# Performance work log

Measured on AMD Instinct MI355X. Metric: run time of the kernel, lower is better.

Reference implementation:

```python
import jax, jax.numpy as jnp
from jax import lax
import numpy as np

EPS = 1e-5
NEG_SLOPE = 0.1
POOL = 2


def _cond_block(x, w, b, fcw, fcb, g, be, rm, rv):
    """CondConv1d(k=3,pad=1,num_experts=e) + BatchNorm1d(eval) + LeakyReLU(0.1).
    x: (B, Cin, W); w: (E, Cout, Cin, 3); b: (E, Cout); fcw: (E, Cin); fcb: (E,)
    """
    # routing: adaptive avg pool to 1 -> fc -> sigmoid  => (B, E)
    r = jax.nn.sigmoid(x.mean(axis=-1) @ fcw.T + fcb)
    # per-sample mixed weights/bias
    cw = jnp.einsum('be,eoik->boik', r, w)          # (B, Cout, Cin, 3)
    cb = r @ b                                      # (B, Cout)
    # batched per-sample conv1d (same padding, stride 1)
    def one(xi, wi):
        return lax.conv_general_dilated(
            xi[None], wi, window_strides=(1,), padding=[(1, 1)],
            dimension_numbers=('NCH', 'OIH', 'NCH'))[0]
    y = jax.vmap(one)(x, cw) + cb[:, :, None]       # (B, Cout, W)
    # BatchNorm1d in eval mode (running stats)
    y = (y - rm[None, :, None]) * (g[None, :, None] / jnp.sqrt(rv[None, :, None] + EPS)) + be[None, :, None]
    # LeakyReLU(0.1)
    return jnp.where(y >= 0, y, NEG_SLOPE * y)


def setup_inputs() -> dict:
    key = jax.random.key(0)
    ks = jax.random.split(key, 16)
    B, W = 32, 2048
    chans = [64, 128, 256]
    E = 1  # num_experts default
    inp = {'x': jax.random.normal(ks[0], (B, chans[0], W), dtype=jnp.float32)}
    i = 1
    for li, (ci, co) in enumerate(zip(chans[:-1], chans[1:]), start=1):
        fan_in = ci * 3
        wb = float(np.sqrt(6.0 / fan_in))  # kaiming_uniform a=sqrt(5) scale approx
        bb = float(1.0 / np.sqrt(fan_in))
        inp[f'w{li}'] = jax.random.uniform(ks[i], (E, co, ci, 3), minval=-wb, maxval=wb, dtype=jnp.float32); i += 1
        inp[f'b{li}'] = jax.random.uniform(ks[i], (E, co), minval=-bb, maxval=bb, dtype=jnp.float32); i += 1
        inp[f'fcw{li}'] = jax.random.normal(ks[i], (E, ci), dtype=jnp.float32) * 0.05; i += 1
        inp[f'fcb{li}'] = jnp.zeros((E,), dtype=jnp.float32)
        inp[f'g{li}'] = 1.0 + 0.1 * jax.random.normal(ks[i], (co,), dtype=jnp.float32); i += 1
        inp[f'be{li}'] = 0.1 * jax.random.normal(ks[i], (co,), dtype=jnp.float32); i += 1
        inp[f'rm{li}'] = 0.1 * jax.random.normal(ks[i], (co,), dtype=jnp.float32); i += 1
        inp[f'rv{li}'] = 0.5 + jax.random.uniform(ks[i], (co,), dtype=jnp.float32); i += 1
    return inp


def reference(x, w1, b1, fcw1, fcb1, g1, be1, rm1, rv1,
              w2, b2, fcw2, fcb2, g2, be2, rm2, rv2):
    y = _cond_block(x, w1, b1, fcw1, fcb1, g1, be1, rm1, rv1)
    y = _cond_block(y, w2, b2, fcw2, fcb2, g2, be2, rm2, rv2)
    # max_pool1d(kernel=stride=POOL)
    B, C, W = y.shape
    y = y.reshape(B, C, W // POOL, POOL).max(axis=-1)
    # dropout: eval mode -> identity
    return y
```

## Files before the change

kernel.cpp:

```cpp
#include <hip/hip_runtime.h>
#include <hip/hip_bf16.h>
#include <math.h>

#define BATCH 32
#define WLEN  2048

typedef __attribute__((ext_vector_type(8))) short short8;
typedef __attribute__((ext_vector_type(4))) short short4v;
typedef __attribute__((ext_vector_type(4))) float floatx4;

__device__ inline short f2bf(float f) {
  unsigned u = __float_as_uint(f);
  unsigned r = (u + 0x7fffu + ((u >> 16) & 1u)) >> 16;
  return (short)r;
}

__global__ __launch_bounds__(256) void fused_prep(
    const float* __restrict__ w1, const float* __restrict__ w2,
    const float* __restrict__ x, const float* __restrict__ fcw1,
    short* __restrict__ wp1, short* __restrict__ wp2,
    float* __restrict__ racc1) {
  const int blk = blockIdx.x;
  const int tid = threadIdx.x;
  if (blk < 12) {
    int iw = blk * 256 + tid;
    int o = iw & 127;
    int t = iw >> 7;
    int ig = t & 7;
    int k = t >> 3;
    short8 v;
#pragma unroll
    for (int e = 0; e < 8; ++e) v[e] = f2bf(w1[(o * 64 + ig * 8 + e) * 3 + k]);
    *(short8*)(wp1 + (size_t)iw * 8) = v;
  } else if (blk < 60) {
    int iw = (blk - 12) * 256 + tid;
    int o = iw & 255;
    int t = iw >> 8;
    int ig = t & 15;
    int k = t >> 4;
    short8 v;
#pragma unroll
    for (int e = 0; e < 8; ++e) v[e] = f2bf(w2[(o * 128 + ig * 8 + e) * 3 + k]);
    *(short8*)(wp2 + (size_t)iw * 8) = v;
  } else {
    int t = blk - 60;
    int j = t & 7, b = t >> 3;
    const float4* xb = (const float4*)(x + ((size_t)b * 64 + j * 8) * WLEN);
    float sum = 0.f;
    for (int idx = tid; idx < 8 * 512; idx += 256) {
      int c = idx >> 9;
      float4 v = xb[idx];
      sum += (v.x + v.y + v.z + v.w) * fcw1[j * 8 + c];
    }
    __shared__ float red[256];
    red[tid] = sum;
    __syncthreads();
    for (int s = 128; s > 0; s >>= 1) {
      if (tid < s) red[tid] += red[tid + s];
      __syncthreads();
    }
    if (tid == 0) racc1[b * 8 + j] = red[0];
  }
}

__global__ __launch_bounds__(512) void conv1_mfma(
    const float* __restrict__ x, const short* __restrict__ wp1,
    const float* __restrict__ bias, const float* __restrict__ g,
    const float* __restrict__ be, const float* __restrict__ rm,
    const float* __restrict__ rv, const float* __restrict__ racc1,
    const float* __restrict__ fcb, const float* __restrict__ fcw2,
    short* __restrict__ y1p, float* __restrict__ racc2) {
  const int b = blockIdx.y;
  const int w_base = blockIdx.x * 128;
  const int tid = threadIdx.x;
  const int wave = tid >> 6, lane = tid & 63;
  const int ln = lane & 15, kg = lane >> 4;
  const int oh = wave & 1, wq = wave >> 1;

  __shared__ short xs[8 * 130 * 8];
  __shared__ float red[512];

  const float* xb = x + (size_t)b * 64 * WLEN;
  for (int idx = tid; idx < 8 * 130; idx += 512) {
    int ig = idx / 130;
    int p = idx - ig * 130;
    int w = w_base - 1 + p;
    short8 v = {0, 0, 0, 0, 0, 0, 0, 0};
    if ((unsigned)w < (unsigned)WLEN) {
      const float* src = xb + (size_t)(ig * 8) * WLEN + w;
#pragma unroll
      for (int e = 0; e < 8; ++e) v[e] = f2bf(src[(size_t)e * WLEN]);
    }
    *(short8*)(xs + idx * 8) = v;
  }
  __syncthreads();

  floatx4 acc[4][2];
#pragma unroll
  for (int ms = 0; ms < 4; ++ms)
#pragma unroll
    for (int ns = 0; ns < 2; ++ns) acc[ms][ns] = (floatx4){0.f, 0.f, 0.f, 0.f};

#pragma unroll
  for (int q = 0; q < 2; ++q) {
#pragma unroll
    for (int k = 0; k < 3; ++k) {
      short8 af[4];
      const short* wk =
          wp1 + ((size_t)(k * 8 + q * 4 + kg) * 128 + oh * 64 + ln) * 8;
#pragma unroll
      for (int ms = 0; ms < 4; ++ms)
        af[ms] = *(const short8*)(wk + (size_t)ms * 16 * 8);
#pragma unroll
      for (int ns = 0; ns < 2; ++ns) {
        short8 bf = *(const short8*)(
            xs + ((q * 4 + kg) * 130 + wq * 32 + ns * 16 + ln + k) * 8);
#pragma unroll
        for (int ms = 0; ms < 4; ++ms)
          acc[ms][ns] = __builtin_amdgcn_mfma_f32_16x16x32_bf16(
              af[ms], bf, acc[ms][ns], 0, 0, 0);
      }
    }
  }

  float zs = 0.f;
#pragma unroll
  for (int qq = 0; qq < 8; ++qq) zs += racc1[b * 8 + qq];
  float z = zs * (1.f / (float)WLEN) + fcb[0];
  float r = 1.f / (1.f + expf(-z));

  float rsum = 0.f;
#pragma unroll
  for (int ms = 0; ms < 4; ++ms) {
    const int o0 = oh * 64 + ms * 16 + kg * 4;
    float a_[4], c_[4], fw[4];
#pragma unroll
    for (int rr = 0; rr < 4; ++rr) {
      int o = o0 + rr;
      float s = g[o] * rsqrtf(rv[o] + 1e-5f);
      a_[rr] = r * s;
      c_[rr] = (r * bias[o] - rm[o]) * s + be[o];
      fw[rr] = fcw2[o];
    }
#pragma unroll
    for (int ns = 0; ns < 2; ++ns) {
      int w = w_base + wq * 32 + ns * 16 + ln;
      short4v pk;
#pragma unroll
      for (int rr = 0; rr < 4; ++rr) {
        float v = acc[ms][ns][rr] * a_[rr] + c_[rr];
        v = v >= 0.f ? v : 0.1f * v;
        rsum += v * fw[rr];
        pk[rr] = f2bf(v);
      }
      *(short4v*)(y1p + ((size_t)(b * 32 + (o0 >> 2)) * WLEN + w) * 4) = pk;
    }
  }

  red[tid] = rsum;
  __syncthreads();
  for (int s = 256; s > 0; s >>= 1) {
    if (tid < s) red[tid] += red[tid + s];
    __syncthreads();
  }
  if (tid == 0) racc2[b * 16 + blockIdx.x] = red[0];
}

__global__ __launch_bounds__(512) void conv2_mfma(
    const short* __restrict__ y1p, const short* __restrict__ wp2,
    const float* __restrict__ bias, const float* __restrict__ g,
    const float* __restrict__ be, const float* __restrict__ rm,
    const float* __restrict__ rv, const float* __restrict__ racc2,
    const float* __restrict__ fcb, float* __restrict__ out) {
  const int b = blockIdx.y;
  const int w_base = blockIdx.x * 128;
  const int tid = threadIdx.x;
  const int wave = tid >> 6, lane = tid & 63;
  const int ln = lane & 15, kg = lane >> 4;
  const int oq = wave & 3, wh = wave >> 2;

  __shared__ short xs[16 * 130 * 8];

  const short* yb = y1p + (size_t)b * 32 * WLEN * 4;
  for (int idx = tid; idx < 16 * 130; idx += 512) {
    int ig = idx / 130;
    int p = idx - ig * 130;
    int w = w_base - 1 + p;
    short8 v = {0, 0, 0, 0, 0, 0, 0, 0};
    if ((unsigned)w < (unsigned)WLEN) {
      short4v a = *(const short4v*)(yb + ((size_t)(ig * 2) * WLEN + w) * 4);
      short4v c = *(const short4v*)(yb + ((size_t)(ig * 2 + 1) * WLEN + w) * 4);
      v[0] = a[0]; v[1] = a[1]; v[2] = a[2]; v[3] = a[3];
      v[4] = c[0]; v[5] = c[1]; v[6] = c[2]; v[7] = c[3];
    }
    *(short8*)(xs + idx * 8) = v;
  }
  __syncthreads();

  floatx4 acc[4][4];
#pragma unroll
  for (int ms = 0; ms < 4; ++ms)
#pragma unroll
    for (int ns = 0; ns < 4; ++ns) acc[ms][ns] = (floatx4){0.f, 0.f, 0.f, 0.f};

#pragma unroll
  for (int q = 0; q < 4; ++q) {
#pragma unroll
    for (int k = 0; k < 3; ++k) {
      short8 af[4];
      const short* wk =
          wp2 + ((size_t)(k * 16 + q * 4 + kg) * 256 + oq * 64 + ln) * 8;
#pragma unroll
      for (int ms = 0; ms < 4; ++ms)
        af[ms] = *(const short8*)(wk + (size_t)ms * 16 * 8);
#pragma unroll
      for (int ns = 0; ns < 4; ++ns) {
        short8 bf = *(const short8*)(
            xs + ((q * 4 + kg) * 130 + wh * 64 + ns * 16 + ln + k) * 8);
#pragma unroll
        for (int ms = 0; ms < 4; ++ms)
          acc[ms][ns] = __builtin_amdgcn_mfma_f32_16x16x32_bf16(
              af[ms], bf, acc[ms][ns], 0, 0, 0);
      }
    }
  }

  float zs = 0.f;
#pragma unroll
  for (int t = 0; t < 16; ++t) zs += racc2[b * 16 + t];
  float z = zs * (1.f / (float)WLEN) + fcb[0];
  float r = 1.f / (1.f + expf(-z));

#pragma unroll
  for (int ms = 0; ms < 4; ++ms) {
    const int o0 = oq * 64 + ms * 16 + kg * 4;
    float a_[4], c_[4];
#pragma unroll
    for (int rr = 0; rr < 4; ++rr) {
      int o = o0 + rr;
      float s = g[o] * rsqrtf(rv[o] + 1e-5f);
      a_[rr] = r * s;
      c_[rr] = (r * bias[o] - rm[o]) * s + be[o];
    }
#pragma unroll
    for (int np = 0; np < 2; ++np) {
      float m0[4], m1[4];
#pragma unroll
      for (int half = 0; half < 2; ++half) {
        int ns = np * 2 + half;
#pragma unroll
        for (int rr = 0; rr < 4; ++rr) {
          float v = acc[ms][ns][rr] * a_[rr] + c_[rr];
          v = v >= 0.f ? v : 0.1f * v;
          float m = fmaxf(v, __shfl_xor(v, 1));
          if (half == 0) m0[rr] = m; else m1[rr] = m;
        }
      }
      const int pc = (w_base >> 1) + wh * 32 + np * 16 + ln;
#pragma unroll
      for (int rr = 0; rr < 4; ++rr) {
        int src = kg * 16 + ((ln & 7) << 1);
        float aa = __shfl(m0[rr], src);
        float bb = __shfl(m1[rr], src);
        float val = (ln < 8) ? aa : bb;
        out[((size_t)(b * 256 + o0 + rr)) * (WLEN / 2) + pc] = val;
      }
    }
  }
}

extern "C" void kernel_launch(void* const* d_in, const int* in_sizes, int n_in,
                              void* d_out, int out_size, void* d_ws, size_t ws_size,
                              hipStream_t stream) {
  const float* x    = (const float*)d_in[0];
  const float* w1   = (const float*)d_in[1];
  const float* b1   = (const float*)d_in[2];
  const float* fcw1 = (const float*)d_in[3];
  const float* fcb1 = (const float*)d_in[4];
  const float* g1   = (const float*)d_in[5];
  const float* be1  = (const float*)d_in[6];
  const float* rm1  = (const float*)d_in[7];
  const float* rv1  = (const float*)d_in[8];
  const float* w2   = (const float*)d_in[9];
  const float* b2   = (const float*)d_in[10];
  const float* fcw2 = (const float*)d_in[11];
  const float* fcb2 = (const float*)d_in[12];
  const float* g2   = (const float*)d_in[13];
  const float* be2  = (const float*)d_in[14];
  const float* rm2  = (const float*)d_in[15];
  const float* rv2  = (const float*)d_in[16];

  float* out = (float*)d_out;

  char* ws = (char*)d_ws;
  short* y1p = (short*)ws;
  short* wp1 = (short*)(ws + (size_t)16 * 1024 * 1024);
  short* wp2 = (short*)(ws + (size_t)16 * 1024 * 1024 + 64 * 1024);
  float* racc1 = (float*)(ws + (size_t)16 * 1024 * 1024 + 512 * 1024);
  float* racc2 = racc1 + 256;

  fused_prep<<<316, 256, 0, stream>>>(w1, w2, x, fcw1, wp1, wp2, racc1);
  conv1_mfma<<<dim3(16, 32), 512, 0, stream>>>(
      x, wp1, b1, g1, be1, rm1, rv1, racc1, fcb1, fcw2, y1p, racc2);
  conv2_mfma<<<dim3(16, 32), 512, 0, stream>>>(
      y1p, wp2, b2, g2, be2, rm2, rv2, racc2, fcb2, out);
}
```

Before: 57.54 us.

## Fuse prep and both conv stages into one cooperative kernel with grid syncs

```diff
diff --git a/kernel.cpp b/kernel.cpp
--- a/kernel.cpp
+++ b/kernel.cpp
@@ -1,6 +1,9 @@
 #include <hip/hip_runtime.h>
 #include <hip/hip_bf16.h>
+#include <hip/hip_cooperative_groups.h>
 #include <math.h>
+
+namespace cg = cooperative_groups;
 
 #define BATCH 32
 #define WLEN  2048
@@ -13,6 +16,273 @@
   unsigned u = __float_as_uint(f);
   unsigned r = (u + 0x7fffu + ((u >> 16) & 1u)) >> 16;
   return (short)r;
+}
+
+__global__ __launch_bounds__(512) void fused_all(
+    const float* __restrict__ x,
+    const float* __restrict__ w1, const float* __restrict__ b1,
+    const float* __restrict__ fcw1, const float* __restrict__ fcb1,
+    const float* __restrict__ g1, const float* __restrict__ be1,
+    const float* __restrict__ rm1, const float* __restrict__ rv1,
+    const float* __restrict__ w2, const float* __restrict__ b2,
+    const float* __restrict__ fcw2, const float* __restrict__ fcb2,
+    const float* __restrict__ g2, const float* __restrict__ be2,
+    const float* __restrict__ rm2, const float* __restrict__ rv2,
+    short* __restrict__ wp1, short* __restrict__ wp2,
+    float* __restrict__ racc1, float* __restrict__ racc2,
+    short* __restrict__ edges, float* __restrict__ out) {
+  const int j = blockIdx.x;
+  const int b = blockIdx.y;
+  const int bid = b * 8 + j;
+  const int tid = threadIdx.x;
+  const int wave = tid >> 6, lane = tid & 63;
+  const int ln = lane & 15, kg = lane >> 4;
+
+  __shared__ short buf[2][16640];
+  __shared__ float red[512];
+
+  cg::grid_group grid = cg::this_grid();
+
+  if (bid < 6) {
+    int iw = bid * 512 + tid;
+    int o = iw & 127;
+    int tt = iw >> 7;
+    int ig = tt & 7;
+    int k = tt >> 3;
+    short8 v;
+#pragma unroll
+    for (int e = 0; e < 8; ++e) v[e] = f2bf(w1[(o * 64 + ig * 8 + e) * 3 + k]);
+    *(short8*)(wp1 + (size_t)iw * 8) = v;
+  } else if (bid < 30) {
+    int iw = (bid - 6) * 512 + tid;
+    int o = iw & 255;
+    int tt = iw >> 8;
+    int ig = tt & 15;
+    int k = tt >> 4;
+    short8 v;
+#pragma unroll
+    for (int e = 0; e < 8; ++e) v[e] = f2bf(w2[(o * 128 + ig * 8 + e) * 3 + k]);
+    *(short8*)(wp2 + (size_t)iw * 8) = v;
+  }
+
+  {
+    const float* xb = x + (size_t)b * 64 * WLEN;
+    float rsum = 0.f;
+#pragma unroll
+    for (int u = 0; u < 2; ++u) {
+      const int w0 = j * 256 + u * 128;
+      for (int idx = tid; idx < 8 * 130; idx += 512) {
+        int ig = idx / 130;
+        int p = idx - ig * 130;
+        int w = w0 - 1 + p;
+        short8 v = {0, 0, 0, 0, 0, 0, 0, 0};
+        if ((unsigned)w < (unsigned)WLEN) {
+          const float* src = xb + (size_t)(ig * 8) * WLEN + w;
+          float fv[8];
+#pragma unroll
+          for (int e = 0; e < 8; ++e) fv[e] = src[(size_t)e * WLEN];
+#pragma unroll
+          for (int e = 0; e < 8; ++e) v[e] = f2bf(fv[e]);
+          if (p >= 1 && p <= 128) {
+#pragma unroll
+            for (int e = 0; e < 8; ++e) rsum += fv[e] * fcw1[ig * 8 + e];
+          }
+        }
+        *(short8*)(buf[u] + (size_t)idx * 8) = v;
+      }
+    }
+    red[tid] = rsum;
+    __syncthreads();
+    for (int s = 256; s > 0; s >>= 1) {
+      if (tid < s) red[tid] += red[tid + s];
+      __syncthreads();
+    }
+    if (tid == 0) racc1[bid] = red[0];
+  }
+  __threadfence();
+  grid.sync();
+
+  {
+    float zs = 0.f;
+#pragma unroll
+    for (int tt = 0; tt < 8; ++tt) zs += racc1[b * 8 + tt];
+    float z = zs * (1.f / (float)WLEN) + fcb1[0];
+    float r1v = 1.f / (1.f + expf(-z));
+
+    const int oh = wave & 1, wq = wave >> 1;
+    float rsum2 = 0.f;
+#pragma unroll
+    for (int u = 0; u < 2; ++u) {
+      floatx4 acc[4][2];
+#pragma unroll
+      for (int ms = 0; ms < 4; ++ms)
+#pragma unroll
+        for (int ns = 0; ns < 2; ++ns) acc[ms][ns] = (floatx4){0.f, 0.f, 0.f, 0.f};
+
+#pragma unroll
+      for (int q = 0; q < 2; ++q) {
+#pragma unroll
+        for (int k = 0; k < 3; ++k) {
+          short8 af[4];
+          const short* wk =
+              wp1 + ((size_t)(k * 8 + q * 4 + kg) * 128 + oh * 64 + ln) * 8;
+#pragma unroll
+          for (int ms = 0; ms < 4; ++ms)
+            af[ms] = *(const short8*)(wk + (size_t)ms * 16 * 8);
+#pragma unroll
+          for (int ns = 0; ns < 2; ++ns) {
+            short8 bf = *(const short8*)(
+                buf[u] + ((q * 4 + kg) * 130 + wq * 32 + ns * 16 + ln + k) * 8);
+#pragma unroll
+            for (int ms = 0; ms < 4; ++ms)
+              acc[ms][ns] = __builtin_amdgcn_mfma_f32_16x16x32_bf16(
+                  af[ms], bf, acc[ms][ns], 0, 0, 0);
+          }
+        }
+      }
+      __syncthreads();
+
+#pragma unroll
+      for (int ms = 0; ms < 4; ++ms) {
+        const int o0 = oh * 64 + ms * 16 + kg * 4;
+        float a_[4], c_[4], fw[4];
+#pragma unroll
+        for (int rr = 0; rr < 4; ++rr) {
+          int o = o0 + rr;
+          float s = g1[o] * rsqrtf(rv1[o] + 1e-5f);
+          a_[rr] = r1v * s;
+          c_[rr] = (r1v * b1[o] - rm1[o]) * s + be1[o];
+          fw[rr] = fcw2[o];
+        }
+#pragma unroll
+        for (int ns = 0; ns < 2; ++ns) {
+          int lw = wq * 32 + ns * 16 + ln;
+          short4v pk;
+#pragma unroll
+          for (int rr = 0; rr < 4; ++rr) {
+            float v = acc[ms][ns][rr] * a_[rr] + c_[rr];
+            v = v >= 0.f ? v : 0.1f * v;
+            rsum2 += v * fw[rr];
+            pk[rr] = f2bf(v);
+          }
+          *(short4v*)(buf[u] + ((o0 >> 3) * 130 + 1 + lw) * 8 + (o0 & 7)) = pk;
+          if (u == 0 && lw == 0)
+            *(short4v*)(edges + ((size_t)bid * 2 + 0) * 128 + o0) = pk;
+          if (u == 1 && lw == 127)
+            *(short4v*)(edges + ((size_t)bid * 2 + 1) * 128 + o0) = pk;
+        }
+      }
+      __syncthreads();
+    }
+    red[tid] = rsum2;
+    __syncthreads();
+    for (int s = 256; s > 0; s >>= 1) {
+      if (tid < s) red[tid] += red[tid + s];
+      __syncthreads();
+    }
+    if (tid == 0) racc2[bid] = red[0];
+  }
+  __threadfence();
+  grid.sync();
+
+  {
+    if (tid < 128) {
+      int c = tid;
+      short v = 0;
+      if (j > 0) v = edges[((size_t)(bid - 1) * 2 + 1) * 128 + c];
+      buf[0][((c >> 3) * 130 + 0) * 8 + (c & 7)] = v;
+    } else if (tid < 256) {
+      int c = tid - 128;
+      buf[0][((c >> 3) * 130 + 129) * 8 + (c & 7)] =
+          buf[1][((c >> 3) * 130 + 1) * 8 + (c & 7)];
+    } else if (tid < 384) {
+      int c = tid - 256;
+      buf[1][((c >> 3) * 130 + 0) * 8 + (c & 7)] =
+          buf[0][((c >> 3) * 130 + 128) * 8 + (c & 7)];
+    } else {
+      int c = tid - 384;
+      short v = 0;
+      if (j < 7) v = edges[((size_t)(bid + 1) * 2 + 0) * 128 + c];
+      buf[1][((c >> 3) * 130 + 129) * 8 + (c & 7)] = v;
+    }
+    __syncthreads();
+
+    float zs = 0.f;
+#pragma unroll
+    for (int tt = 0; tt < 8; ++tt) zs += racc2[b * 8 + tt];
+    float z = zs * (1.f / (float)WLEN) + fcb2[0];
+    float r2v = 1.f / (1.f + expf(-z));
+
+    const int oq = wave & 3, wh = wave >> 2;
+#pragma unroll
+    for (int u = 0; u < 2; ++u) {
+      floatx4 acc[4][4];
+#pragma unroll
+      for (int ms = 0; ms < 4; ++ms)
+#pragma unroll
+        for (int ns = 0; ns < 4; ++ns) acc[ms][ns] = (floatx4){0.f, 0.f, 0.f, 0.f};
+
+#pragma unroll
+      for (int q = 0; q < 4; ++q) {
+#pragma unroll
+        for (int k = 0; k < 3; ++k) {
+          short8 af[4];
+          const short* wk =
+              wp2 + ((size_t)(k * 16 + q * 4 + kg) * 256 + oq * 64 + ln) * 8;
+#pragma unroll
+          for (int ms = 0; ms < 4; ++ms)
+            af[ms] = *(const short8*)(wk + (size_t)ms * 16 * 8);
+#pragma unroll
+          for (int ns = 0; ns < 4; ++ns) {
+            short8 bf = *(const short8*)(
+                buf[u] + ((q * 4 + kg) * 130 + wh * 64 + ns * 16 + ln + k) * 8);
+#pragma unroll
+            for (int ms = 0; ms < 4; ++ms)
+              acc[ms][ns] = __builtin_amdgcn_mfma_f32_16x16x32_bf16(
+                  af[ms], bf, acc[ms][ns], 0, 0, 0);
+          }
+        }
+      }
+
+      const int w0 = j * 256 + u * 128;
+#pragma unroll
+      for (int ms = 0; ms < 4; ++ms) {
+        const int o0 = oq * 64 + ms * 16 + kg * 4;
+        float a_[4], c_[4];
+#pragma unroll
+        for (int rr = 0; rr < 4; ++rr) {
+          int o = o0 + rr;
+          float s = g2[o] * rsqrtf(rv2[o] + 1e-5f);
+          a_[rr] = r2v * s;
+          c_[rr] = (r2v * b2[o] - rm2[o]) * s + be2[o];
+        }
+#pragma unroll
+        for (int np = 0; np < 2; ++np) {
+          float m0[4], m1[4];
+#pragma unroll
+          for (int half = 0; half < 2; ++half) {
+            int ns = np * 2 + half;
+#pragma unroll
+            for (int rr = 0; rr < 4; ++rr) {
+              float v = acc[ms][ns][rr] * a_[rr] + c_[rr];
+              v = v >= 0.f ? v : 0.1f * v;
+              float m = fmaxf(v, __shfl_xor(v, 1));
+              if (half == 0) m0[rr] = m; else m1[rr] = m;
+            }
+          }
+          const int pc = (w0 >> 1) + wh * 32 + np * 16 + ln;
+#pragma unroll
+          for (int rr = 0; rr < 4; ++rr) {
+            int src = kg * 16 + ((ln & 7) << 1);
+            float aa = __shfl(m0[rr], src);
+            float bb = __shfl(m1[rr], src);
+            float val = (ln < 8) ? aa : bb;
+            out[((size_t)(b * 256 + o0 + rr)) * (WLEN / 2) + pc] = val;
+          }
+        }
+      }
+    }
+  }
 }
 
 __global__ __launch_bounds__(256) void fused_prep(
@@ -44,13 +314,13 @@
     *(short8*)(wp2 + (size_t)iw * 8) = v;
   } else {
     int t = blk - 60;
-    int j = t & 7, b = t >> 3;
-    const float4* xb = (const float4*)(x + ((size_t)b * 64 + j * 8) * WLEN);
+    int jj = t & 7, b = t >> 3;
+    const float4* xb = (const float4*)(x + ((size_t)b * 64 + jj * 8) * WLEN);
     float sum = 0.f;
     for (int idx = tid; idx < 8 * 512; idx += 256) {
       int c = idx >> 9;
       float4 v = xb[idx];
-      sum += (v.x + v.y + v.z + v.w) * fcw1[j * 8 + c];
+      sum += (v.x + v.y + v.z + v.w) * fcw1[jj * 8 + c];
     }
     __shared__ float red[256];
     red[tid] = sum;
@@ -59,11 +329,11 @@
       if (tid < s) red[tid] += red[tid + s];
       __syncthreads();
     }
-    if (tid == 0) racc1[b * 8 + j] = red[0];
+    if (tid == 0) racc1[b * 8 + jj] = red[0];
   }
 }
 
-__global__ __launch_bounds__(512) void conv1_mfma(
+__global__ __launch_bounds__(512) void fb_conv1(
     const float* __restrict__ x, const short* __restrict__ wp1,
     const float* __restrict__ bias, const float* __restrict__ g,
     const float* __restrict__ be, const float* __restrict__ rm,
@@ -127,9 +397,9 @@
 #pragma unroll
   for (int qq = 0; qq < 8; ++qq) zs += racc1[b * 8 + qq];
   float z = zs * (1.f / (float)WLEN) + fcb[0];
-  float r = 1.f / (1.f + expf(-z));
-
-  float rsum = 0.f;
+  float r1v = 1.f / (1.f + expf(-z));
+
+  float rsum2 = 0.f;
 #pragma unroll
   for (int ms = 0; ms < 4; ++ms) {
     const int o0 = oh * 64 + ms * 16 + kg * 4;
@@ -138,26 +408,25 @@
     for (int rr = 0; rr < 4; ++rr) {
       int o = o0 + rr;
       float s = g[o] * rsqrtf(rv[o] + 1e-5f);
-      a_[rr] = r * s;
-      c_[rr] = (r * bias[o] - rm[o]) * s + be[o];
+      a_[rr] = r1v * s;
+      c_[rr] = (r1v * bias[o] - rm[o]) * s + be[o];
       fw[rr] = fcw2[o];
     }
 #pragma unroll
     for (int ns = 0; ns < 2; ++ns) {
-      int w = w_base + wq * 32 + ns * 16 + ln;
+      int lw = wq * 32 + ns * 16 + ln;
       short4v pk;
 #pragma unroll
       for (int rr = 0; rr < 4; ++rr) {
         float v = acc[ms][ns][rr] * a_[rr] + c_[rr];
         v = v >= 0.f ? v : 0.1f * v;
-        rsum += v * fw[rr];
+        rsum2 += v * fw[rr];
         pk[rr] = f2bf(v);
       }
-      *(short4v*)(y1p + ((size_t)(b * 32 + (o0 >> 2)) * WLEN + w) * 4) = pk;
-    }
-  }
-
-  red[tid] = rsum;
+      *(short4v*)(y1p + ((size_t)(b * 32 + (o0 >> 2)) * WLEN + w_base + lw) * 4) = pk;
+    }
+  }
+  red[tid] = rsum2;
   __syncthreads();
   for (int s = 256; s > 0; s >>= 1) {
     if (tid < s) red[tid] += red[tid + s];
@@ -166,7 +435,7 @@
   if (tid == 0) racc2[b * 16 + blockIdx.x] = red[0];
 }
 
-__global__ __launch_bounds__(512) void conv2_mfma(
+__global__ __launch_bounds__(512) void fb_conv2(
     const short* __restrict__ y1p, const short* __restrict__ wp2,
     const float* __restrict__ bias, const float* __restrict__ g,
     const float* __restrict__ be, const float* __restrict__ rm,
@@ -229,7 +498,7 @@
 #pragma unroll
   for (int t = 0; t < 16; ++t) zs += racc2[b * 16 + t];
   float z = zs * (1.f / (float)WLEN) + fcb[0];
-  float r = 1.f / (1.f + expf(-z));
+  float r2v = 1.f / (1.f + expf(-z));
 
 #pragma unroll
   for (int ms = 0; ms < 4; ++ms) {
@@ -239,8 +508,8 @@
     for (int rr = 0; rr < 4; ++rr) {
       int o = o0 + rr;
       float s = g[o] * rsqrtf(rv[o] + 1e-5f);
-      a_[rr] = r * s;
-      c_[rr] = (r * bias[o] - rm[o]) * s + be[o];
+      a_[rr] = r2v * s;
+      c_[rr] = (r2v * bias[o] - rm[o]) * s + be[o];
     }
 #pragma unroll
     for (int np = 0; np < 2; ++np) {
@@ -289,19 +558,33 @@
   const float* be2  = (const float*)d_in[14];
   const float* rm2  = (const float*)d_in[15];
   const float* rv2  = (const float*)d_in[16];
-
   float* out = (float*)d_out;
 
   char* ws = (char*)d_ws;
-  short* y1p = (short*)ws;
-  short* wp1 = (short*)(ws + (size_t)16 * 1024 * 1024);
-  short* wp2 = (short*)(ws + (size_t)16 * 1024 * 1024 + 64 * 1024);
-  float* racc1 = (float*)(ws + (size_t)16 * 1024 * 1024 + 512 * 1024);
-  float* racc2 = racc1 + 256;
-
-  fused_prep<<<316, 256, 0, stream>>>(w1, w2, x, fcw1, wp1, wp2, racc1);
-  conv1_mfma<<<dim3(16, 32), 512, 0, stream>>>(
-      x, wp1, b1, g1, be1, rm1, rv1, racc1, fcb1, fcw2, y1p, racc2);
-  conv2_mfma<<<dim3(16, 32), 512, 0, stream>>>(
-      y1p, wp2, b2, g2, be2, rm2, rv2, racc2, fcb2, out);
+  short* wp1   = (short*)(ws);
+  short* wp2   = (short*)(ws + 65536);
+  float* racc1 = (float*)(ws + 262144);
+  float* racc2 = (float*)(ws + 264192);
+  short* edges = (short*)(ws + 266240);
+  short* y1p   = (short*)(ws + (size_t)1024 * 1024);
+
+  void* args[] = {
+      (void*)&x,
+      (void*)&w1, (void*)&b1, (void*)&fcw1, (void*)&fcb1,
+      (void*)&g1, (void*)&be1, (void*)&rm1, (void*)&rv1,
+      (void*)&w2, (void*)&b2, (void*)&fcw2, (void*)&fcb2,
+      (void*)&g2, (void*)&be2, (void*)&rm2, (void*)&rv2,
+      (void*)&wp1, (void*)&wp2, (void*)&racc1, (void*)&racc2,
+      (void*)&edges, (void*)&out};
+
+  hipError_t err = hipLaunchCooperativeKernel(
+      (const void*)fused_all, dim3(8, 32), dim3(512), args, 0, stream);
+  if (err != hipSuccess) {
+    (void)hipGetLastError();
+    fused_prep<<<316, 256, 0, stream>>>(w1, w2, x, fcw1, wp1, wp2, racc1);
+    fb_conv1<<<dim3(16, 32), 512, 0, stream>>>(
+        x, wp1, b1, g1, be1, rm1, rv1, racc1, fcb1, fcw2, y1p, racc2);
+    fb_conv2<<<dim3(16, 32), 512, 0, stream>>>(
+        y1p, wp2, b2, g2, be2, rm2, rv2, racc2, fcb2, out);
+  }
 }
```

Measured after the change: 189.0 us. +228.4%, slower.

## Halve width tiles to double grid and store conv1 output in 8-channel packs

Applied to the files above, without the earlier changes.

```diff
diff --git a/kernel.cpp b/kernel.cpp
--- a/kernel.cpp
+++ b/kernel.cpp
@@ -63,7 +63,7 @@
   }
 }
 
-__global__ __launch_bounds__(512) void conv1_mfma(
+__global__ __launch_bounds__(256) void conv1_mfma(
     const float* __restrict__ x, const short* __restrict__ wp1,
     const float* __restrict__ bias, const float* __restrict__ g,
     const float* __restrict__ be, const float* __restrict__ rm,
@@ -71,20 +71,21 @@
     const float* __restrict__ fcb, const float* __restrict__ fcw2,
     short* __restrict__ y1p, float* __restrict__ racc2) {
   const int b = blockIdx.y;
-  const int w_base = blockIdx.x * 128;
+  const int wt = blockIdx.x;
+  const int w0 = wt * 64;
   const int tid = threadIdx.x;
   const int wave = tid >> 6, lane = tid & 63;
   const int ln = lane & 15, kg = lane >> 4;
   const int oh = wave & 1, wq = wave >> 1;
 
-  __shared__ short xs[8 * 130 * 8];
-  __shared__ float red[512];
+  __shared__ short xs[8 * 66 * 8];
+  __shared__ float red[256];
 
   const float* xb = x + (size_t)b * 64 * WLEN;
-  for (int idx = tid; idx < 8 * 130; idx += 512) {
-    int ig = idx / 130;
-    int p = idx - ig * 130;
-    int w = w_base - 1 + p;
+  for (int idx = tid; idx < 8 * 66; idx += 256) {
+    int ig = idx / 66;
+    int p = idx - ig * 66;
+    int w = w0 - 1 + p;
     short8 v = {0, 0, 0, 0, 0, 0, 0, 0};
     if ((unsigned)w < (unsigned)WLEN) {
       const float* src = xb + (size_t)(ig * 8) * WLEN + w;
@@ -114,7 +115,7 @@
 #pragma unroll
       for (int ns = 0; ns < 2; ++ns) {
         short8 bf = *(const short8*)(
-            xs + ((q * 4 + kg) * 130 + wq * 32 + ns * 16 + ln + k) * 8);
+            xs + ((q * 4 + kg) * 66 + wq * 32 + ns * 16 + ln + k) * 8);
 #pragma unroll
         for (int ms = 0; ms < 4; ++ms)
           acc[ms][ns] = __builtin_amdgcn_mfma_f32_16x16x32_bf16(
@@ -127,9 +128,9 @@
 #pragma unroll
   for (int qq = 0; qq < 8; ++qq) zs += racc1[b * 8 + qq];
   float z = zs * (1.f / (float)WLEN) + fcb[0];
-  float r = 1.f / (1.f + expf(-z));
-
-  float rsum = 0.f;
+  float r1v = 1.f / (1.f + expf(-z));
+
+  float rsum2 = 0.f;
 #pragma unroll
   for (int ms = 0; ms < 4; ++ms) {
     const int o0 = oh * 64 + ms * 16 + kg * 4;
@@ -138,32 +139,31 @@
     for (int rr = 0; rr < 4; ++rr) {
       int o = o0 + rr;
       float s = g[o] * rsqrtf(rv[o] + 1e-5f);
-      a_[rr] = r * s;
-      c_[rr] = (r * bias[o] - rm[o]) * s + be[o];
+      a_[rr] = r1v * s;
+      c_[rr] = (r1v * bias[o] - rm[o]) * s + be[o];
       fw[rr] = fcw2[o];
     }
 #pragma unroll
     for (int ns = 0; ns < 2; ++ns) {
-      int w = w_base + wq * 32 + ns * 16 + ln;
+      int w = w0 + wq * 32 + ns * 16 + ln;
       short4v pk;
 #pragma unroll
       for (int rr = 0; rr < 4; ++rr) {
         float v = acc[ms][ns][rr] * a_[rr] + c_[rr];
         v = v >= 0.f ? v : 0.1f * v;
-        rsum += v * fw[rr];
+        rsum2 += v * fw[rr];
         pk[rr] = f2bf(v);
       }
-      *(short4v*)(y1p + ((size_t)(b * 32 + (o0 >> 2)) * WLEN + w) * 4) = pk;
-    }
-  }
-
-  red[tid] = rsum;
+      *(short4v*)(y1p + ((size_t)(b * 16 + (o0 >> 3)) * WLEN + w) * 8 + (o0 & 7)) = pk;
+    }
+  }
+  red[tid] = rsum2;
   __syncthreads();
-  for (int s = 256; s > 0; s >>= 1) {
+  for (int s = 128; s > 0; s >>= 1) {
     if (tid < s) red[tid] += red[tid + s];
     __syncthreads();
   }
-  if (tid == 0) racc2[b * 16 + blockIdx.x] = red[0];
+  if (tid == 0) racc2[b * 32 + wt] = red[0];
 }
 
 __global__ __launch_bounds__(512) void conv2_mfma(
@@ -173,35 +173,31 @@
     const float* __restrict__ rv, const float* __restrict__ racc2,
     const float* __restrict__ fcb, float* __restrict__ out) {
   const int b = blockIdx.y;
-  const int w_base = blockIdx.x * 128;
+  const int w0 = blockIdx.x * 64;
   const int tid = threadIdx.x;
   const int wave = tid >> 6, lane = tid & 63;
   const int ln = lane & 15, kg = lane >> 4;
   const int oq = wave & 3, wh = wave >> 2;
 
-  __shared__ short xs[16 * 130 * 8];
-
-  const short* yb = y1p + (size_t)b * 32 * WLEN * 4;
-  for (int idx = tid; idx < 16 * 130; idx += 512) {
-    int ig = idx / 130;
-    int p = idx - ig * 130;
-    int w = w_base - 1 + p;
+  __shared__ short xs[16 * 66 * 8];
+
+  const short* yb = y1p + (size_t)b * 16 * WLEN * 8;
+  for (int idx = tid; idx < 16 * 66; idx += 512) {
+    int ig = idx / 66;
+    int p = idx - ig * 66;
+    int w = w0 - 1 + p;
     short8 v = {0, 0, 0, 0, 0, 0, 0, 0};
-    if ((unsigned)w < (unsigned)WLEN) {
-      short4v a = *(const short4v*)(yb + ((size_t)(ig * 2) * WLEN + w) * 4);
-      short4v c = *(const short4v*)(yb + ((size_t)(ig * 2 + 1) * WLEN + w) * 4);
-      v[0] = a[0]; v[1] = a[1]; v[2] = a[2]; v[3] = a[3];
-      v[4] = c[0]; v[5] = c[1]; v[6] = c[2]; v[7] = c[3];
-    }
+    if ((unsigned)w < (unsigned)WLEN)
+      v = *(const short8*)(yb + ((size_t)ig * WLEN + w) * 8);
     *(short8*)(xs + idx * 8) = v;
   }
   __syncthreads();
 
-  floatx4 acc[4][4];
+  floatx4 acc[4][2];
 #pragma unroll
   for (int ms = 0; ms < 4; ++ms)
 #pragma unroll
-    for (int ns = 0; ns < 4; ++ns) acc[ms][ns] = (floatx4){0.f, 0.f, 0.f, 0.f};
+    for (int ns = 0; ns < 2; ++ns) acc[ms][ns] = (floatx4){0.f, 0.f, 0.f, 0.f};
 
 #pragma unroll
   for (int q = 0; q < 4; ++q) {
@@ -214,9 +210,9 @@
       for (int ms = 0; ms < 4; ++ms)
         af[ms] = *(const short8*)(wk + (size_t)ms * 16 * 8);
 #pragma unroll
-      for (int ns = 0; ns < 4; ++ns) {
+      for (int ns = 0; ns < 2; ++ns) {
         short8 bf = *(const short8*)(
-            xs + ((q * 4 + kg) * 130 + wh * 64 + ns * 16 + ln + k) * 8);
+            xs + ((q * 4 + kg) * 66 + wh * 32 + ns * 16 + ln + k) * 8);
 #pragma unroll
         for (int ms = 0; ms < 4; ++ms)
           acc[ms][ns] = __builtin_amdgcn_mfma_f32_16x16x32_bf16(
@@ -227,9 +223,9 @@
 
   float zs = 0.f;
 #pragma unroll
-  for (int t = 0; t < 16; ++t) zs += racc2[b * 16 + t];
+  for (int t = 0; t < 32; ++t) zs += racc2[b * 32 + t];
   float z = zs * (1.f / (float)WLEN) + fcb[0];
-  float r = 1.f / (1.f + expf(-z));
+  float r2v = 1.f / (1.f + expf(-z));
 
 #pragma unroll
   for (int ms = 0; ms < 4; ++ms) {
@@ -239,32 +235,28 @@
     for (int rr = 0; rr < 4; ++rr) {
       int o = o0 + rr;
       float s = g[o] * rsqrtf(rv[o] + 1e-5f);
-      a_[rr] = r * s;
-      c_[rr] = (r * bias[o] - rm[o]) * s + be[o];
-    }
-#pragma unroll
-    for (int np = 0; np < 2; ++np) {
-      float m0[4], m1[4];
-#pragma unroll
-      for (int half = 0; half < 2; ++half) {
-        int ns = np * 2 + half;
-#pragma unroll
-        for (int rr = 0; rr < 4; ++rr) {
-          float v = acc[ms][ns][rr] * a_[rr] + c_[rr];
-          v = v >= 0.f ? v : 0.1f * v;
-          float m = fmaxf(v, __shfl_xor(v, 1));
-          if (half == 0) m0[rr] = m; else m1[rr] = m;
-        }
-      }
-      const int pc = (w_base >> 1) + wh * 32 + np * 16 + ln;
+      a_[rr] = r2v * s;
+      c_[rr] = (r2v * bias[o] - rm[o]) * s + be[o];
+    }
+    float m0[4], m1[4];
+#pragma unroll
+    for (int half = 0; half < 2; ++half) {
 #pragma unroll
       for (int rr = 0; rr < 4; ++rr) {
-        int src = kg * 16 + ((ln & 7) << 1);
-        float aa = __shfl(m0[rr], src);
-        float bb = __shfl(m1[rr], src);
-        float val = (ln < 8) ? aa : bb;
-        out[((size_t)(b * 256 + o0 + rr)) * (WLEN / 2) + pc] = val;
-      }
+        float v = acc[ms][half][rr] * a_[rr] + c_[rr];
+        v = v >= 0.f ? v : 0.1f * v;
+        float m = fmaxf(v, __shfl_xor(v, 1));
+        if (half == 0) m0[rr] = m; else m1[rr] = m;
+      }
+    }
+    const int pc = (w0 >> 1) + wh * 16 + ln;
+#pragma unroll
+    for (int rr = 0; rr < 4; ++rr) {
+      int src = kg * 16 + ((ln & 7) << 1);
+      float aa = __shfl(m0[rr], src);
+      float bb = __shfl(m1[rr], src);
+      float val = (ln < 8) ? aa : bb;
+      out[((size_t)(b * 256 + o0 + rr)) * (WLEN / 2) + pc] = val;
     }
   }
 }
@@ -289,19 +281,18 @@
   const float* be2  = (const float*)d_in[14];
   const float* rm2  = (const float*)d_in[15];
   const float* rv2  = (const float*)d_in[16];
-
   float* out = (float*)d_out;
 
   char* ws = (char*)d_ws;
-  short* y1p = (short*)ws;
-  short* wp1 = (short*)(ws + (size_t)16 * 1024 * 1024);
-  short* wp2 = (short*)(ws + (size_t)16 * 1024 * 1024 + 64 * 1024);
-  float* racc1 = (float*)(ws + (size_t)16 * 1024 * 1024 + 512 * 1024);
+  short* y1p   = (short*)ws;
+  short* wp1   = (short*)(ws + (size_t)16 * 1024 * 1024);
+  short* wp2   = (short*)(ws + (size_t)16 * 1024 * 1024 + 65536);
+  float* racc1 = (float*)(ws + (size_t)16 * 1024 * 1024 + 327680);
   float* racc2 = racc1 + 256;
 
   fused_prep<<<316, 256, 0, stream>>>(w1, w2, x, fcw1, wp1, wp2, racc1);
-  conv1_mfma<<<dim3(16, 32), 512, 0, stream>>>(
+  conv1_mfma<<<dim3(32, 32), 256, 0, stream>>>(
       x, wp1, b1, g1, be1, rm1, rv1, racc1, fcb1, fcw2, y1p, racc2);
-  conv2_mfma<<<dim3(16, 32), 512, 0, stream>>>(
+  conv2_mfma<<<dim3(32, 32), 512, 0, stream>>>(
       y1p, wp2, b2, g2, be2, rm2, rv2, racc2, fcb2, out);
 }
```

Result: faster. 55.94 us (-2.8%).
